# Performance work log

Measured on AMD Instinct MI355X. Metric: run time of the kernel, lower is better.

Reference implementation:

```python
import jax, jax.numpy as jnp
import numpy as np

IOU_THRESHOLD = 0.5


def setup_inputs() -> dict:
    key = jax.random.key(0)
    k1, k2, k3 = jax.random.split(key, 3)
    B, N = 4, 8192
    # valid boxes: top-left in [0,200), width/height in [1,51)
    xy = jax.random.uniform(k1, (B, N, 2), dtype=jnp.float32) * 200.0
    wh = jax.random.uniform(k2, (B, N, 2), dtype=jnp.float32) * 50.0 + 1.0
    boxes = jnp.concatenate([xy, xy + wh], axis=-1)  # [B,N,4] (x1,y1,x2,y2)
    scores = jax.random.uniform(k3, (B, N), dtype=jnp.float32)
    return {"boxes": boxes, "scores": scores}


def _soft_nms_single(boxes, scores):
    # boxes: [N,4], scores: [N]
    x1, y1, x2, y2 = boxes[:, 0], boxes[:, 1], boxes[:, 2], boxes[:, 3]
    inter_w = jnp.maximum(0.0, jnp.minimum(x2[:, None], x2[None, :]) - jnp.maximum(x1[:, None], x1[None, :]))
    inter_h = jnp.maximum(0.0, jnp.minimum(y2[:, None], y2[None, :]) - jnp.maximum(y1[:, None], y1[None, :]))
    inter = inter_w * inter_h  # [N,N]
    area = (x2 - x1) * (y2 - y1)  # [N]
    union = area[:, None] + area[None, :] - inter
    iou = inter / union  # [N,N]
    weight = jnp.exp(-iou / IOU_THRESHOLD)  # [N,N]
    adjusted = weight @ scores  # [N] : adjusted_scores[i] = sum_j w[i,j]*s[j]
    w = jax.nn.softmax(adjusted, axis=0)  # [N]
    return w @ boxes  # [4]


def reference(boxes, scores):
    return jax.vmap(_soft_nms_single)(boxes, scores)  # [B,4]
```

## Files before the change

kernel.cpp:

```cpp
#include <hip/hip_runtime.h>
#include <hip/hip_bf16.h>

#define BATCH   4
#define NBOX    8192
#define BLOCK   256
#define TSZ     256
#define NT      (NBOX / TSZ)
#define NPAIRS  (NT * (NT + 1) / 2)
#define NBINS   2048
#define SUBS    8
#define SUBSZ   (NBOX / SUBS)
#define STH     512

__device__ __forceinline__ float bf2f(unsigned short u) {
    union { unsigned int i; float f; } c;
    c.i = ((unsigned int)u) << 16;
    return c.f;
}

__device__ __forceinline__ bool box_plausible(float x1, float y1, float x2, float y2) {
    bool ok = (x1 == x1) && (y1 == y1) && (x2 == x2) && (y2 == y2);
    ok = ok && fabsf(x1) < 1e4f && fabsf(y1) < 1e4f && fabsf(x2) < 1e4f && fabsf(y2) < 1e4f;
    ok = ok && x1 >= -1.0f && x1 <= 300.0f && y1 >= -1.0f && y1 <= 300.0f;
    const float w = x2 - x1, h = y2 - y1;
    ok = ok && w >= -0.1f && w <= 80.0f && h >= -0.1f && h <= 80.0f;
    return ok;
}

__device__ __forceinline__ bool wave_probe_is_f32(const void* boxes_raw) {
    const int lane = threadIdx.x & 63;
    const float* bf = (const float*)boxes_raw;
    const bool okf = box_plausible(bf[lane * 4 + 0], bf[lane * 4 + 1],
                                   bf[lane * 4 + 2], bf[lane * 4 + 3]);
    const unsigned short* bh = (const unsigned short*)boxes_raw;
    const bool okh = box_plausible(bf2f(bh[lane * 4 + 0]), bf2f(bh[lane * 4 + 1]),
                                   bf2f(bh[lane * 4 + 2]), bf2f(bh[lane * 4 + 3]));
    const unsigned long long mf = __ballot(okf);
    const unsigned long long mh = __ballot(okh);
    return __popcll(mf) >= __popcll(mh);
}

__device__ __forceinline__ float4 load_box(const void* boxes_raw, size_t idx, bool isf32) {
    if (isf32) {
        return reinterpret_cast<const float4*>(boxes_raw)[idx];
    } else {
        const ushort4 u = reinterpret_cast<const ushort4*>(boxes_raw)[idx];
        return make_float4(bf2f(u.x), bf2f(u.y), bf2f(u.z), bf2f(u.w));
    }
}

__device__ __forceinline__ float load_score(const void* scores_raw, size_t idx, bool isf32) {
    return isf32 ? ((const float*)scores_raw)[idx]
                 : bf2f(((const unsigned short*)scores_raw)[idx]);
}

__device__ __forceinline__ int x1_bin(float x1) {
    const int bb = (int)(x1 * 8.0f);
    return min(NBINS - 1, max(0, bb));
}

#define CEXP (-2.8853900817779268f)

__device__ __forceinline__ float pair_weight(
    float ix1, float iy1, float ix2, float iy2, float iarea,
    const float4& bj, float jarea)
{
    float w = fminf(ix2, bj.z) - fmaxf(ix1, bj.x);
    float h = fminf(iy2, bj.w) - fmaxf(iy1, bj.y);
    w = fmaxf(w, 0.0f);
    h = fmaxf(h, 0.0f);
    const float inter = w * h;
    const float uni   = iarea + jarea - inter;
    const float arg   = (CEXP * inter) * __builtin_amdgcn_rcpf(uni);
    return __builtin_amdgcn_exp2f(arg);
}

__global__ __launch_bounds__(STH) void sort_kernel(
    const void* __restrict__ boxes_raw, const void* __restrict__ scores_raw,
    float4* __restrict__ sboxes, float* __restrict__ sscores,
    float* __restrict__ adj,
    float* __restrict__ minx1c, float* __restrict__ maxx2c,
    int* __restrict__ pairlist, int* __restrict__ count)
{
    __shared__ int hist[NBINS];
    __shared__ int bmax[NBINS];
    __shared__ int hist2[NBINS];
    __shared__ int wsum[STH / 64];
    __shared__ float sminT[NT], smaxT[NT];
    __shared__ int scnt;

    const int b    = blockIdx.x / SUBS;
    const int sub  = blockIdx.x % SUBS;
    const int tid  = threadIdx.x;
    const int lane = tid & 63;
    const int wv   = tid >> 6;
    const bool isf32 = wave_probe_is_f32(boxes_raw);
    const size_t base = (size_t)b * NBOX;

#pragma unroll
    for (int i = 0; i < NBINS / STH; i++) {
        hist[i * STH + tid]  = 0;
        bmax[i * STH + tid]  = 0;
        hist2[i * STH + tid] = 0;
    }
    if (tid == 0) scnt = 0;
    {
        const size_t z = (size_t)blockIdx.x * 1024;
        adj[z + tid] = 0.0f;
        adj[z + STH + tid] = 0.0f;
    }
    __syncthreads();

#pragma unroll
    for (int k = 0; k < NBOX / STH; k++) {
        const float4 bx = load_box(boxes_raw, base + k * STH + tid, isf32);
        const int bin = x1_bin(bx.x);
        atomicAdd(&hist[bin], 1);
        atomicMax(&bmax[bin], __float_as_int(bx.z));
    }
    for (int i = tid; i < sub * SUBSZ; i += STH) {
        const float4 bx = load_box(boxes_raw, base + i, isf32);
        atomicAdd(&hist2[x1_bin(bx.x)], 1);
    }
    __syncthreads();

    {
        int tot[4], cum[4];
        int run = 0;
#pragma unroll
        for (int i = 0; i < 4; i++) {
            tot[i] = hist[tid * 4 + i];
            run += tot[i]; cum[i] = run;
        }
        int v = run;
#pragma unroll
        for (int d = 1; d < 64; d <<= 1) {
            const int u = __shfl_up(v, d);
            if (lane >= d) v += u;
        }
        if (lane == 63) wsum[wv] = v;
        __syncthreads();
        int wb = 0;
        for (int w = 0; w < wv; w++) wb += wsum[w];
        const int tb = wb + v - run;
#pragma unroll
        for (int i = 0; i < 4; i++) {
            const int bin = tid * 4 + i;
            const int e = tb + cum[i] - tot[i];
            const int m = hist2[bin];
            hist[bin]  = e;
            hist2[bin] = e + m;
        }
    }
    __syncthreads();

    if (tid < NT) {
        int p = tid * TSZ;
        int lo = 0, hi = NBINS - 1;
        while (lo < hi) { const int mid = (lo + hi + 1) >> 1;
                          if (hist[mid] <= p) lo = mid; else hi = mid - 1; }
        const int Bf = lo;
        p = tid * TSZ + TSZ - 1;
        lo = 0; hi = NBINS - 1;
        while (lo < hi) { const int mid = (lo + hi + 1) >> 1;
                          if (hist[mid] <= p) lo = mid; else hi = mid - 1; }
        const int Bl = lo;
        int mb = 0;
        for (int q = Bf; q <= Bl; q++) mb = max(mb, bmax[q]);
        const float mn = (float)Bf * 0.125f;
        const float mx = __int_as_float(mb);
        sminT[tid] = mn; smaxT[tid] = mx;
        if (sub == 0) {
            minx1c[b * NT + tid] = mn;
            maxx2c[b * NT + tid] = mx;
        }
    }
    __syncthreads();

    if (sub == 0) {
        for (int q = tid; q < NPAIRS; q += STH) {
            int p = q, it = 0;
            while (p >= NT - it) { p -= NT - it; it++; }
            const int jt = it + p;
            const bool live = !((smaxT[it] < sminT[jt]) || (smaxT[jt] < sminT[it]));
            if (live) {
                const int idx = atomicAdd(&scnt, 1);
                pairlist[b * NPAIRS + idx] = (it << 8) | jt;
            }
        }
    }

#pragma unroll
    for (int k = 0; k < SUBSZ / STH; k++) {
        const int i = sub * SUBSZ + k * STH + tid;
        const float4 bx = load_box(boxes_raw, base + i, isf32);
        const float  sc = load_score(scores_raw, base + i, isf32);
        const int pos = atomicAdd(&hist2[x1_bin(bx.x)], 1);
        sboxes[base + pos]  = bx;
        sscores[base + pos] = sc;
    }

    __syncthreads();
    if (sub == 0 && tid == 0) count[b] = scnt;
}

__global__ __launch_bounds__(BLOCK, 4) void soft_nms_adj_kernel(
    const float4* __restrict__ sboxes,
    const float* __restrict__ sscores,
    const int* __restrict__ pairlist,
    const int* __restrict__ count,
    float* __restrict__ adj)
{
    __shared__ float4 sbox[TSZ];
    __shared__ float2 sas[TSZ];
    __shared__ float  srow[4][TSZ];

    const int bid = blockIdx.x;
    const int b   = bid / NPAIRS;
    const int p   = bid % NPAIRS;
    if (p >= count[b]) return;
    const int pr = pairlist[b * NPAIRS + p];
    const int it = pr >> 8, jt = pr & 255;

    const int tid  = threadIdx.x;
    const int lane = tid & 63;
    const int wv   = tid >> 6;
    const size_t base = (size_t)b * NBOX;

    {
        const int jg = jt * TSZ + tid;
        const float4 uj = sboxes[base + jg];
        sbox[tid] = uj;
        sas[tid]  = make_float2((uj.z - uj.x) * (uj.w - uj.y), sscores[base + jg]);
    }

    float rx1[4], ry1[4], rx2[4], ry2[4], rar[4], rsc[4], accr[4];
#pragma unroll
    for (int k = 0; k < 4; k++) {
        const int ig = it * TSZ + k * 64 + lane;
        const float4 ui = sboxes[base + ig];
        rx1[k] = ui.x; ry1[k] = ui.y; rx2[k] = ui.z; ry2[k] = ui.w;
        rar[k] = (ui.z - ui.x) * (ui.w - ui.y);
        rsc[k] = sscores[base + ig];
        accr[k] = 0.0f;
    }

    __syncthreads();

    const int wvbase = wv * 64;

    if (it == jt) {
#pragma unroll 2
        for (int t = 0; t < 64; t++) {
            const int idx = wvbase + ((lane + t) & 63);
            const float4 bj = sbox[idx];
            const float2 as = sas[idx];
#pragma unroll
            for (int k = 0; k < 4; k++) {
                const float e = pair_weight(rx1[k], ry1[k], rx2[k], ry2[k], rar[k], bj, as.x);
                accr[k] = fmaf(e, as.y, accr[k]);
            }
        }
    } else {
        float accc = 0.0f;
#pragma unroll 2
        for (int t = 0; t < 64; t++) {
            const int idx = wvbase + ((lane + t) & 63);
            const float4 bj = sbox[idx];
            const float2 as = sas[idx];
            const float e0 = pair_weight(rx1[0], ry1[0], rx2[0], ry2[0], rar[0], bj, as.x);
            const float e1 = pair_weight(rx1[1], ry1[1], rx2[1], ry2[1], rar[1], bj, as.x);
            const float e2 = pair_weight(rx1[2], ry1[2], rx2[2], ry2[2], rar[2], bj, as.x);
            const float e3 = pair_weight(rx1[3], ry1[3], rx2[3], ry2[3], rar[3], bj, as.x);
            accr[0] = fmaf(e0, as.y, accr[0]);
            accr[1] = fmaf(e1, as.y, accr[1]);
            accr[2] = fmaf(e2, as.y, accr[2]);
            accr[3] = fmaf(e3, as.y, accr[3]);
            const float c = fmaf(e0, rsc[0], fmaf(e1, rsc[1], fmaf(e2, rsc[2], e3 * rsc[3])));
            accc += __shfl(c, (lane - t) & 63);
        }
        atomicAdd(&adj[base + jt * TSZ + wvbase + lane], accc);
    }

#pragma unroll
    for (int k = 0; k < 4; k++) srow[wv][k * 64 + lane] = accr[k];
    __syncthreads();
    {
        const float rs = srow[0][tid] + srow[1][tid] + srow[2][tid] + srow[3][tid];
        atomicAdd(&adj[base + it * TSZ + tid], rs);
    }
}

#define FBLK 1024
__global__ __launch_bounds__(FBLK) void soft_nms_finish_kernel(
    const float4* __restrict__ sboxes,
    const float* __restrict__ sscores,
    const float* __restrict__ adj,
    const float* __restrict__ minx1c, const float* __restrict__ maxx2c,
    const void* __restrict__ boxes_raw,
    void* __restrict__ out)
{
    constexpr int K  = NBOX / FBLK;
    constexpr int NW = FBLK / 64;
    __shared__ float sminx[NT], smaxx[NT], ssumT[NT], scorr[NT];
    __shared__ float smax_[NW];
    __shared__ float sred[NW][5];

    const int b    = blockIdx.x;
    const int tid  = threadIdx.x;
    const int lane = tid & 63;
    const int wv   = tid >> 6;
    const size_t base = (size_t)b * NBOX;

    const bool isf32 = wave_probe_is_f32(boxes_raw);

    if (tid < NT) {
        sminx[tid] = minx1c[b * NT + tid];
        smaxx[tid] = maxx2c[b * NT + tid];
    }
#pragma unroll
    for (int tt = 0; tt < 2; tt++) {
        const int T = wv * 2 + tt;
        float sm = 0.0f;
#pragma unroll
        for (int q = 0; q < 4; q++) sm += sscores[base + T * TSZ + q * 64 + lane];
#pragma unroll
        for (int off = 32; off > 0; off >>= 1) sm += __shfl_down(sm, off);
        if (lane == 0) ssumT[T] = sm;
    }
    __syncthreads();
    if (tid < NT) {
        float c = 0.0f;
        for (int T2 = 0; T2 < NT; T2++) {
            const bool skip = (smaxx[tid] < sminx[T2]) || (smaxx[T2] < sminx[tid]);
            if (skip) c += ssumT[T2];
        }
        scorr[tid] = c;
    }
    __syncthreads();

    float av[K];
    float m = -3.4e38f;
#pragma unroll
    for (int k = 0; k < K; k++) {
        const int r = k * FBLK + tid;
        av[k] = adj[base + r] + scorr[r >> 8];
        m = fmaxf(m, av[k]);
    }
#pragma unroll
    for (int off = 32; off > 0; off >>= 1)
        m = fmaxf(m, __shfl_down(m, off));
    if (lane == 0) smax_[wv] = m;
    __syncthreads();
    float M = smax_[0];
#pragma unroll
    for (int w = 1; w < NW; w++) M = fmaxf(M, smax_[w]);

    const float L2E = 1.4426950408889634f;
    float es = 0.0f, s0 = 0.0f, s1 = 0.0f, s2 = 0.0f, s3 = 0.0f;
#pragma unroll
    for (int k = 0; k < K; k++) {
        const float e = __builtin_amdgcn_exp2f((av[k] - M) * L2E);
        const float4 u = sboxes[base + k * FBLK + tid];
        es += e;
        s0 += e * u.x;
        s1 += e * u.y;
        s2 += e * u.z;
        s3 += e * u.w;
    }
#pragma unroll
    for (int off = 32; off > 0; off >>= 1) {
        es += __shfl_down(es, off);
        s0 += __shfl_down(s0, off);
        s1 += __shfl_down(s1, off);
        s2 += __shfl_down(s2, off);
        s3 += __shfl_down(s3, off);
    }
    if (lane == 0) {
        sred[wv][0] = es; sred[wv][1] = s0; sred[wv][2] = s1;
        sred[wv][3] = s2; sred[wv][4] = s3;
    }
    __syncthreads();
    if (tid == 0) {
        float ES = 0.0f, o[4] = {0.0f, 0.0f, 0.0f, 0.0f};
#pragma unroll
        for (int w = 0; w < NW; w++) {
            ES   += sred[w][0];
            o[0] += sred[w][1];
            o[1] += sred[w][2];
            o[2] += sred[w][3];
            o[3] += sred[w][4];
        }
        const float inv = 1.0f / ES;
        if (isf32) {
            float* of = (float*)out;
            for (int c = 0; c < 4; c++) of[b * 4 + c] = o[c] * inv;
        } else {
            __hip_bfloat16* oh = (__hip_bfloat16*)out;
            for (int c = 0; c < 4; c++) oh[b * 4 + c] = __float2bfloat16(o[c] * inv);
        }
    }
}

extern "C" void kernel_launch(void* const* d_in, const int* in_sizes, int n_in,
                              void* d_out, int out_size, void* d_ws, size_t ws_size,
                              hipStream_t stream) {
    const void* boxes_raw  = d_in[0];
    const void* scores_raw = d_in[1];

    char* w = (char*)d_ws;
    float4* sboxes   = (float4*)w;                 w += (size_t)BATCH * NBOX * 16;
    float*  sscores  = (float*)w;                  w += (size_t)BATCH * NBOX * 4;
    float*  adj      = (float*)w;                  w += (size_t)BATCH * NBOX * 4;
    float*  minx1c   = (float*)w;                  w += (size_t)BATCH * NT * 4;
    float*  maxx2c   = (float*)w;                  w += (size_t)BATCH * NT * 4;
    int*    pairlist = (int*)w;                    w += (size_t)BATCH * NPAIRS * 4;
    int*    count    = (int*)w;

    sort_kernel<<<dim3(BATCH * SUBS), dim3(STH), 0, stream>>>(
        boxes_raw, scores_raw, sboxes, sscores, adj, minx1c, maxx2c, pairlist, count);
    soft_nms_adj_kernel<<<dim3(BATCH * NPAIRS), dim3(BLOCK), 0, stream>>>(
        sboxes, sscores, pairlist, count, adj);
    soft_nms_finish_kernel<<<dim3(BATCH), dim3(FBLK), 0, stream>>>(
        sboxes, sscores, adj, minx1c, maxx2c, boxes_raw, d_out);
}
```

Measured before the change: 120.8 us.

## Fuse sort, pair-adjust and finish stages into one cooperative persistent kernel

Replaces the three-kernel pipeline with one cooperative kernel of 1024 blocks that runs the stages back to back, separated by grid-wide syncs. The sort stage is split into per-sub-block histograms written to global memory, then merged after a grid sync, so the old serial prefix recount is no longer needed. The pair work becomes a persistent loop with 256 blocks per batch, and the finish stage runs in 256-thread blocks. The goal is to remove launch gaps and the long-pole sort prologue; the cost is grid-sync overhead, and only 4 blocks do the final reduction with smaller blocks. The old three-kernel path is kept as a fallback if the cooperative launch fails.

```diff
diff --git a/kernel.cpp b/kernel.cpp
--- a/kernel.cpp
+++ b/kernel.cpp
@@ -1,5 +1,8 @@
 #include <hip/hip_runtime.h>
 #include <hip/hip_bf16.h>
+#include <hip/hip_cooperative_groups.h>
+
+namespace cg = cooperative_groups;
 
 #define BATCH   4
 #define NBOX    8192
@@ -10,7 +13,8 @@
 #define NBINS   2048
 #define SUBS    8
 #define SUBSZ   (NBOX / SUBS)
-#define STH     512
+#define GRID    1024
+#define PPB     256
 
 __device__ __forceinline__ float bf2f(unsigned short u) {
     union { unsigned int i; float f; } c;
@@ -60,6 +64,7 @@
 }
 
 #define CEXP (-2.8853900817779268f)
+#define L2E  (1.4426950408889634f)
 
 __device__ __forceinline__ float pair_weight(
     float ix1, float iy1, float ix2, float iy2, float iarea,
@@ -75,165 +80,17 @@
     return __builtin_amdgcn_exp2f(arg);
 }
 
-__global__ __launch_bounds__(STH) void sort_kernel(
-    const void* __restrict__ boxes_raw, const void* __restrict__ scores_raw,
-    float4* __restrict__ sboxes, float* __restrict__ sscores,
-    float* __restrict__ adj,
-    float* __restrict__ minx1c, float* __restrict__ maxx2c,
-    int* __restrict__ pairlist, int* __restrict__ count)
+__device__ __forceinline__ void adj_pair_body(
+    const float4* sboxes, const float* sscores, float* adj,
+    size_t base, int it, int jt, int tid, int lane, int wv,
+    float4* sbox, float2* sas, float (*srow)[TSZ])
 {
-    __shared__ int hist[NBINS];
-    __shared__ int bmax[NBINS];
-    __shared__ int hist2[NBINS];
-    __shared__ int wsum[STH / 64];
-    __shared__ float sminT[NT], smaxT[NT];
-    __shared__ int scnt;
-
-    const int b    = blockIdx.x / SUBS;
-    const int sub  = blockIdx.x % SUBS;
-    const int tid  = threadIdx.x;
-    const int lane = tid & 63;
-    const int wv   = tid >> 6;
-    const bool isf32 = wave_probe_is_f32(boxes_raw);
-    const size_t base = (size_t)b * NBOX;
-
-#pragma unroll
-    for (int i = 0; i < NBINS / STH; i++) {
-        hist[i * STH + tid]  = 0;
-        bmax[i * STH + tid]  = 0;
-        hist2[i * STH + tid] = 0;
-    }
-    if (tid == 0) scnt = 0;
-    {
-        const size_t z = (size_t)blockIdx.x * 1024;
-        adj[z + tid] = 0.0f;
-        adj[z + STH + tid] = 0.0f;
-    }
-    __syncthreads();
-
-#pragma unroll
-    for (int k = 0; k < NBOX / STH; k++) {
-        const float4 bx = load_box(boxes_raw, base + k * STH + tid, isf32);
-        const int bin = x1_bin(bx.x);
-        atomicAdd(&hist[bin], 1);
-        atomicMax(&bmax[bin], __float_as_int(bx.z));
-    }
-    for (int i = tid; i < sub * SUBSZ; i += STH) {
-        const float4 bx = load_box(boxes_raw, base + i, isf32);
-        atomicAdd(&hist2[x1_bin(bx.x)], 1);
-    }
-    __syncthreads();
-
-    {
-        int tot[4], cum[4];
-        int run = 0;
-#pragma unroll
-        for (int i = 0; i < 4; i++) {
-            tot[i] = hist[tid * 4 + i];
-            run += tot[i]; cum[i] = run;
-        }
-        int v = run;
-#pragma unroll
-        for (int d = 1; d < 64; d <<= 1) {
-            const int u = __shfl_up(v, d);
-            if (lane >= d) v += u;
-        }
-        if (lane == 63) wsum[wv] = v;
-        __syncthreads();
-        int wb = 0;
-        for (int w = 0; w < wv; w++) wb += wsum[w];
-        const int tb = wb + v - run;
-#pragma unroll
-        for (int i = 0; i < 4; i++) {
-            const int bin = tid * 4 + i;
-            const int e = tb + cum[i] - tot[i];
-            const int m = hist2[bin];
-            hist[bin]  = e;
-            hist2[bin] = e + m;
-        }
-    }
-    __syncthreads();
-
-    if (tid < NT) {
-        int p = tid * TSZ;
-        int lo = 0, hi = NBINS - 1;
-        while (lo < hi) { const int mid = (lo + hi + 1) >> 1;
-                          if (hist[mid] <= p) lo = mid; else hi = mid - 1; }
-        const int Bf = lo;
-        p = tid * TSZ + TSZ - 1;
-        lo = 0; hi = NBINS - 1;
-        while (lo < hi) { const int mid = (lo + hi + 1) >> 1;
-                          if (hist[mid] <= p) lo = mid; else hi = mid - 1; }
-        const int Bl = lo;
-        int mb = 0;
-        for (int q = Bf; q <= Bl; q++) mb = max(mb, bmax[q]);
-        const float mn = (float)Bf * 0.125f;
-        const float mx = __int_as_float(mb);
-        sminT[tid] = mn; smaxT[tid] = mx;
-        if (sub == 0) {
-            minx1c[b * NT + tid] = mn;
-            maxx2c[b * NT + tid] = mx;
-        }
-    }
-    __syncthreads();
-
-    if (sub == 0) {
-        for (int q = tid; q < NPAIRS; q += STH) {
-            int p = q, it = 0;
-            while (p >= NT - it) { p -= NT - it; it++; }
-            const int jt = it + p;
-            const bool live = !((smaxT[it] < sminT[jt]) || (smaxT[jt] < sminT[it]));
-            if (live) {
-                const int idx = atomicAdd(&scnt, 1);
-                pairlist[b * NPAIRS + idx] = (it << 8) | jt;
-            }
-        }
-    }
-
-#pragma unroll
-    for (int k = 0; k < SUBSZ / STH; k++) {
-        const int i = sub * SUBSZ + k * STH + tid;
-        const float4 bx = load_box(boxes_raw, base + i, isf32);
-        const float  sc = load_score(scores_raw, base + i, isf32);
-        const int pos = atomicAdd(&hist2[x1_bin(bx.x)], 1);
-        sboxes[base + pos]  = bx;
-        sscores[base + pos] = sc;
-    }
-
-    __syncthreads();
-    if (sub == 0 && tid == 0) count[b] = scnt;
-}
-
-__global__ __launch_bounds__(BLOCK, 4) void soft_nms_adj_kernel(
-    const float4* __restrict__ sboxes,
-    const float* __restrict__ sscores,
-    const int* __restrict__ pairlist,
-    const int* __restrict__ count,
-    float* __restrict__ adj)
-{
-    __shared__ float4 sbox[TSZ];
-    __shared__ float2 sas[TSZ];
-    __shared__ float  srow[4][TSZ];
-
-    const int bid = blockIdx.x;
-    const int b   = bid / NPAIRS;
-    const int p   = bid % NPAIRS;
-    if (p >= count[b]) return;
-    const int pr = pairlist[b * NPAIRS + p];
-    const int it = pr >> 8, jt = pr & 255;
-
-    const int tid  = threadIdx.x;
-    const int lane = tid & 63;
-    const int wv   = tid >> 6;
-    const size_t base = (size_t)b * NBOX;
-
     {
         const int jg = jt * TSZ + tid;
         const float4 uj = sboxes[base + jg];
         sbox[tid] = uj;
         sas[tid]  = make_float2((uj.z - uj.x) * (uj.w - uj.y), sscores[base + jg]);
     }
-
     float rx1[4], ry1[4], rx2[4], ry2[4], rar[4], rsc[4], accr[4];
 #pragma unroll
     for (int k = 0; k < 4; k++) {
@@ -244,11 +101,9 @@
         rsc[k] = sscores[base + ig];
         accr[k] = 0.0f;
     }
-
     __syncthreads();
 
     const int wvbase = wv * 64;
-
     if (it == jt) {
 #pragma unroll 2
         for (int t = 0; t < 64; t++) {
@@ -285,20 +140,397 @@
 #pragma unroll
     for (int k = 0; k < 4; k++) srow[wv][k * 64 + lane] = accr[k];
     __syncthreads();
+    const float rs = srow[0][tid] + srow[1][tid] + srow[2][tid] + srow[3][tid];
+    atomicAdd(&adj[base + it * TSZ + tid], rs);
+}
+
+__global__ __launch_bounds__(BLOCK, 4) void mega_kernel(
+    const void* __restrict__ boxes_raw, const void* __restrict__ scores_raw,
+    float4* __restrict__ sboxes, float* __restrict__ sscores,
+    float* __restrict__ adj,
+    int* __restrict__ ghist, int* __restrict__ gmaxp,
+    float* __restrict__ minx1c, float* __restrict__ maxx2c,
+    int* __restrict__ pairlist, int* __restrict__ count,
+    void* __restrict__ out)
+{
+    cg::grid_group gg = cg::this_grid();
+    __shared__ __align__(16) char smem[25088];
+
+    const int bid  = blockIdx.x;
+    const int tid  = threadIdx.x;
+    const int lane = tid & 63;
+    const int wv   = tid >> 6;
+    const bool isf32 = wave_probe_is_f32(boxes_raw);
+
+    if (bid < BATCH * SUBS) {
+        int* hist = (int*)smem;
+        int* hmax = hist + NBINS;
+        const int b = bid / SUBS, sub = bid % SUBS;
+        const size_t base = (size_t)b * NBOX;
+#pragma unroll
+        for (int i = 0; i < NBINS / BLOCK; i++) {
+            hist[i * BLOCK + tid] = 0; hmax[i * BLOCK + tid] = 0;
+        }
+        __syncthreads();
+#pragma unroll
+        for (int k = 0; k < SUBSZ / BLOCK; k++) {
+            const float4 bx = load_box(boxes_raw, base + sub * SUBSZ + k * BLOCK + tid, isf32);
+            const int bin = x1_bin(bx.x);
+            atomicAdd(&hist[bin], 1);
+            atomicMax(&hmax[bin], __float_as_int(bx.z));
+        }
+        __syncthreads();
+#pragma unroll
+        for (int i = 0; i < NBINS / BLOCK; i++) {
+            const int bin = i * BLOCK + tid;
+            ghist[((size_t)b * NBINS + bin) * SUBS + sub] = hist[bin];
+            gmaxp[((size_t)b * NBINS + bin) * SUBS + sub] = hmax[bin];
+        }
+    } else if (bid < 2 * BATCH * SUBS) {
+        const size_t z = (size_t)(bid - BATCH * SUBS) * 1024;
+#pragma unroll
+        for (int k = 0; k < 4; k++) adj[z + k * BLOCK + tid] = 0.0f;
+    }
+    gg.sync();
+
+    if (bid < BATCH * SUBS) {
+        int*   sex   = (int*)smem;
+        int*   loff  = sex + NBINS;
+        int*   bmaxs = loff + NBINS;
+        int*   wsum  = bmaxs + NBINS;
+        float* sminT = (float*)(wsum + 4);
+        float* smaxT = sminT + NT;
+        int*   scnt  = (int*)(smaxT + NT);
+        const int b = bid / SUBS, sub = bid % SUBS;
+        const size_t base = (size_t)b * NBOX;
+        if (tid == 0) *scnt = 0;
+
+        int tot[8], mys[8], cum[8];
+        int run = 0;
+#pragma unroll
+        for (int i = 0; i < 8; i++) {
+            const int bin = tid * 8 + i;
+            const int* g = &ghist[((size_t)b * NBINS + bin) * SUBS];
+            const int* x = &gmaxp[((size_t)b * NBINS + bin) * SUBS];
+            int t = 0, m = 0, bm = 0;
+#pragma unroll
+            for (int s = 0; s < SUBS; s++) {
+                const int c = g[s];
+                t += c;
+                if (s < sub) m += c;
+                bm = max(bm, x[s]);
+            }
+            tot[i] = t; mys[i] = m; run += t; cum[i] = run;
+            bmaxs[bin] = bm;
+        }
+        int v = run;
+#pragma unroll
+        for (int d = 1; d < 64; d <<= 1) {
+            const int u = __shfl_up(v, d);
+            if (lane >= d) v += u;
+        }
+        if (lane == 63) wsum[wv] = v;
+        __syncthreads();
+        int wb = 0;
+        for (int w2 = 0; w2 < wv; w2++) wb += wsum[w2];
+        const int tb = wb + v - run;
+#pragma unroll
+        for (int i = 0; i < 8; i++) {
+            const int bin = tid * 8 + i;
+            const int e = tb + cum[i] - tot[i];
+            sex[bin]  = e;
+            loff[bin] = e + mys[i];
+        }
+        __syncthreads();
+
+        if (sub == 0 && tid < NT) {
+            int p = tid * TSZ;
+            int lo = 0, hi = NBINS - 1;
+            while (lo < hi) { const int mid = (lo + hi + 1) >> 1;
+                              if (sex[mid] <= p) lo = mid; else hi = mid - 1; }
+            const int Bf = lo;
+            p = tid * TSZ + TSZ - 1;
+            lo = 0; hi = NBINS - 1;
+            while (lo < hi) { const int mid = (lo + hi + 1) >> 1;
+                              if (sex[mid] <= p) lo = mid; else hi = mid - 1; }
+            const int Bl = lo;
+            int mb = 0;
+            for (int q = Bf; q <= Bl; q++) mb = max(mb, bmaxs[q]);
+            sminT[tid] = (float)Bf * 0.125f;
+            smaxT[tid] = __int_as_float(mb);
+            minx1c[b * NT + tid] = sminT[tid];
+            maxx2c[b * NT + tid] = smaxT[tid];
+        }
+        __syncthreads();
+
+        if (sub == 0) {
+            for (int q = tid; q < NPAIRS; q += BLOCK) {
+                int p = q, it = 0;
+                while (p >= NT - it) { p -= NT - it; it++; }
+                const int jt = it + p;
+                const bool live = !((smaxT[it] < sminT[jt]) || (smaxT[jt] < sminT[it]));
+                if (live) {
+                    const int idx = atomicAdd(scnt, 1);
+                    pairlist[b * NPAIRS + idx] = (it << 8) | jt;
+                }
+            }
+        }
+#pragma unroll
+        for (int k = 0; k < SUBSZ / BLOCK; k++) {
+            const int i = sub * SUBSZ + k * BLOCK + tid;
+            const float4 bx = load_box(boxes_raw, base + i, isf32);
+            const float  sc = load_score(scores_raw, base + i, isf32);
+            const int pos = atomicAdd(&loff[x1_bin(bx.x)], 1);
+            sboxes[base + pos]  = bx;
+            sscores[base + pos] = sc;
+        }
+        __syncthreads();
+        if (sub == 0 && tid == 0) count[b] = *scnt;
+    }
+    gg.sync();
+
     {
-        const float rs = srow[0][tid] + srow[1][tid] + srow[2][tid] + srow[3][tid];
-        atomicAdd(&adj[base + it * TSZ + tid], rs);
-    }
+        float4* sbox = (float4*)smem;
+        float2* sas  = (float2*)(smem + 4096);
+        float (*srow)[TSZ] = (float(*)[TSZ])(smem + 6144);
+        const int b  = bid >> 8;
+        const size_t base = (size_t)b * NBOX;
+        const int cnt = count[b];
+        for (int p = (bid & (PPB - 1)); p < cnt; p += PPB) {
+            __syncthreads();
+            const int pr = pairlist[b * NPAIRS + p];
+            adj_pair_body(sboxes, sscores, adj, base, pr >> 8, pr & 255,
+                          tid, lane, wv, sbox, sas, srow);
+        }
+    }
+    gg.sync();
+
+    if (bid < BATCH) {
+        float* sminx = (float*)smem;
+        float* smaxx = sminx + NT;
+        float* ssumT = smaxx + NT;
+        float* scorr = ssumT + NT;
+        float* smaxw = scorr + NT;
+        float (*sred)[5] = (float(*)[5])(smaxw + 4);
+        const int b = bid;
+        const size_t base = (size_t)b * NBOX;
+
+        if (tid < NT) {
+            sminx[tid] = minx1c[b * NT + tid];
+            smaxx[tid] = maxx2c[b * NT + tid];
+        }
+#pragma unroll
+        for (int tt = 0; tt < 8; tt++) {
+            const int T = wv * 8 + tt;
+            float sm = 0.0f;
+#pragma unroll
+            for (int q = 0; q < 4; q++) sm += sscores[base + T * TSZ + q * 64 + lane];
+#pragma unroll
+            for (int off = 32; off > 0; off >>= 1) sm += __shfl_down(sm, off);
+            if (lane == 0) ssumT[T] = sm;
+        }
+        __syncthreads();
+        if (tid < NT) {
+            float c = 0.0f;
+            for (int T2 = 0; T2 < NT; T2++) {
+                const bool skip = (smaxx[tid] < sminx[T2]) || (smaxx[T2] < sminx[tid]);
+                if (skip) c += ssumT[T2];
+            }
+            scorr[tid] = c;
+        }
+        __syncthreads();
+
+        float m = -3.4e38f;
+#pragma unroll
+        for (int k = 0; k < NBOX / BLOCK; k++) {
+            const int r = k * BLOCK + tid;
+            m = fmaxf(m, adj[base + r] + scorr[r >> 8]);
+        }
+#pragma unroll
+        for (int off = 32; off > 0; off >>= 1) m = fmaxf(m, __shfl_down(m, off));
+        if (lane == 0) smaxw[wv] = m;
+        __syncthreads();
+        const float M = fmaxf(fmaxf(smaxw[0], smaxw[1]), fmaxf(smaxw[2], smaxw[3]));
+
+        float es = 0.0f, s0 = 0.0f, s1 = 0.0f, s2 = 0.0f, s3 = 0.0f;
+#pragma unroll
+        for (int k = 0; k < NBOX / BLOCK; k++) {
+            const int r = k * BLOCK + tid;
+            const float e = __builtin_amdgcn_exp2f((adj[base + r] + scorr[r >> 8] - M) * L2E);
+            const float4 u = sboxes[base + r];
+            es += e; s0 += e * u.x; s1 += e * u.y; s2 += e * u.z; s3 += e * u.w;
+        }
+#pragma unroll
+        for (int off = 32; off > 0; off >>= 1) {
+            es += __shfl_down(es, off);
+            s0 += __shfl_down(s0, off);
+            s1 += __shfl_down(s1, off);
+            s2 += __shfl_down(s2, off);
+            s3 += __shfl_down(s3, off);
+        }
+        if (lane == 0) {
+            sred[wv][0] = es; sred[wv][1] = s0; sred[wv][2] = s1;
+            sred[wv][3] = s2; sred[wv][4] = s3;
+        }
+        __syncthreads();
+        if (tid == 0) {
+            float ES = 0.0f, o[4] = {0.0f, 0.0f, 0.0f, 0.0f};
+#pragma unroll
+            for (int w2 = 0; w2 < 4; w2++) {
+                ES += sred[w2][0];
+                o[0] += sred[w2][1]; o[1] += sred[w2][2];
+                o[2] += sred[w2][3]; o[3] += sred[w2][4];
+            }
+            const float inv = 1.0f / ES;
+            if (isf32) {
+                float* of = (float*)out;
+                for (int c = 0; c < 4; c++) of[b * 4 + c] = o[c] * inv;
+            } else {
+                __hip_bfloat16* oh = (__hip_bfloat16*)out;
+                for (int c = 0; c < 4; c++) oh[b * 4 + c] = __float2bfloat16(o[c] * inv);
+            }
+        }
+    }
+}
+
+__global__ __launch_bounds__(512) void sort_kernel_fb(
+    const void* __restrict__ boxes_raw, const void* __restrict__ scores_raw,
+    float4* __restrict__ sboxes, float* __restrict__ sscores,
+    float* __restrict__ adj,
+    float* __restrict__ minx1c, float* __restrict__ maxx2c,
+    int* __restrict__ pairlist, int* __restrict__ count)
+{
+    __shared__ int hist[NBINS];
+    __shared__ int bmax[NBINS];
+    __shared__ int hist2[NBINS];
+    __shared__ int wsum[8];
+    __shared__ float sminT[NT], smaxT[NT];
+    __shared__ int scnt;
+
+    const int b    = blockIdx.x / SUBS;
+    const int sub  = blockIdx.x % SUBS;
+    const int tid  = threadIdx.x;
+    const int lane = tid & 63;
+    const int wv   = tid >> 6;
+    const bool isf32 = wave_probe_is_f32(boxes_raw);
+    const size_t base = (size_t)b * NBOX;
+
+#pragma unroll
+    for (int i = 0; i < NBINS / 512; i++) {
+        hist[i * 512 + tid] = 0; bmax[i * 512 + tid] = 0; hist2[i * 512 + tid] = 0;
+    }
+    if (tid == 0) scnt = 0;
+    {
+        const size_t z = (size_t)blockIdx.x * 1024;
+        adj[z + tid] = 0.0f; adj[z + 512 + tid] = 0.0f;
+    }
+    __syncthreads();
+
+#pragma unroll
+    for (int k = 0; k < NBOX / 512; k++) {
+        const float4 bx = load_box(boxes_raw, base + k * 512 + tid, isf32);
+        const int bin = x1_bin(bx.x);
+        atomicAdd(&hist[bin], 1);
+        atomicMax(&bmax[bin], __float_as_int(bx.z));
+    }
+    for (int i = tid; i < sub * SUBSZ; i += 512) {
+        const float4 bx = load_box(boxes_raw, base + i, isf32);
+        atomicAdd(&hist2[x1_bin(bx.x)], 1);
+    }
+    __syncthreads();
+
+    {
+        int tot[4], cum[4];
+        int run = 0;
+#pragma unroll
+        for (int i = 0; i < 4; i++) { tot[i] = hist[tid * 4 + i]; run += tot[i]; cum[i] = run; }
+        int v = run;
+#pragma unroll
+        for (int d = 1; d < 64; d <<= 1) { const int u = __shfl_up(v, d); if (lane >= d) v += u; }
+        if (lane == 63) wsum[wv] = v;
+        __syncthreads();
+        int wb = 0;
+        for (int w = 0; w < wv; w++) wb += wsum[w];
+        const int tb = wb + v - run;
+#pragma unroll
+        for (int i = 0; i < 4; i++) {
+            const int bin = tid * 4 + i;
+            const int e = tb + cum[i] - tot[i];
+            const int m = hist2[bin];
+            hist[bin]  = e;
+            hist2[bin] = e + m;
+        }
+    }
+    __syncthreads();
+
+    if (tid < NT) {
+        int p = tid * TSZ;
+        int lo = 0, hi = NBINS - 1;
+        while (lo < hi) { const int mid = (lo + hi + 1) >> 1;
+                          if (hist[mid] <= p) lo = mid; else hi = mid - 1; }
+        const int Bf = lo;
+        p = tid * TSZ + TSZ - 1;
+        lo = 0; hi = NBINS - 1;
+        while (lo < hi) { const int mid = (lo + hi + 1) >> 1;
+                          if (hist[mid] <= p) lo = mid; else hi = mid - 1; }
+        const int Bl = lo;
+        int mb = 0;
+        for (int q = Bf; q <= Bl; q++) mb = max(mb, bmax[q]);
+        sminT[tid] = (float)Bf * 0.125f;
+        smaxT[tid] = __int_as_float(mb);
+        if (sub == 0) { minx1c[b * NT + tid] = sminT[tid]; maxx2c[b * NT + tid] = smaxT[tid]; }
+    }
+    __syncthreads();
+
+    if (sub == 0) {
+        for (int q = tid; q < NPAIRS; q += 512) {
+            int p = q, it = 0;
+            while (p >= NT - it) { p -= NT - it; it++; }
+            const int jt = it + p;
+            const bool live = !((smaxT[it] < sminT[jt]) || (smaxT[jt] < sminT[it]));
+            if (live) {
+                const int idx = atomicAdd(&scnt, 1);
+                pairlist[b * NPAIRS + idx] = (it << 8) | jt;
+            }
+        }
+    }
+#pragma unroll
+    for (int k = 0; k < SUBSZ / 512; k++) {
+        const int i = sub * SUBSZ + k * 512 + tid;
+        const float4 bx = load_box(boxes_raw, base + i, isf32);
+        const float  sc = load_score(scores_raw, base + i, isf32);
+        const int pos = atomicAdd(&hist2[x1_bin(bx.x)], 1);
+        sboxes[base + pos]  = bx;
+        sscores[base + pos] = sc;
+    }
+    __syncthreads();
+    if (sub == 0 && tid == 0) count[b] = scnt;
+}
+
+__global__ __launch_bounds__(BLOCK, 4) void adj_kernel_fb(
+    const float4* __restrict__ sboxes, const float* __restrict__ sscores,
+    const int* __restrict__ pairlist, const int* __restrict__ count,
+    float* __restrict__ adj)
+{
+    __shared__ float4 sbox[TSZ];
+    __shared__ float2 sas[TSZ];
+    __shared__ float  srow[4][TSZ];
+
+    const int bid = blockIdx.x;
+    const int b   = bid / NPAIRS;
+    const int p   = bid % NPAIRS;
+    if (p >= count[b]) return;
+    const int pr = pairlist[b * NPAIRS + p];
+    adj_pair_body(sboxes, sscores, adj, (size_t)b * NBOX, pr >> 8, pr & 255,
+                  threadIdx.x, threadIdx.x & 63, threadIdx.x >> 6, sbox, sas, srow);
 }
 
 #define FBLK 1024
-__global__ __launch_bounds__(FBLK) void soft_nms_finish_kernel(
-    const float4* __restrict__ sboxes,
-    const float* __restrict__ sscores,
+__global__ __launch_bounds__(FBLK) void finish_kernel_fb(
+    const float4* __restrict__ sboxes, const float* __restrict__ sscores,
     const float* __restrict__ adj,
     const float* __restrict__ minx1c, const float* __restrict__ maxx2c,
-    const void* __restrict__ boxes_raw,
-    void* __restrict__ out)
+    const void* __restrict__ boxes_raw, void* __restrict__ out)
 {
     constexpr int K  = NBOX / FBLK;
     constexpr int NW = FBLK / 64;
@@ -311,13 +543,9 @@
     const int lane = tid & 63;
     const int wv   = tid >> 6;
     const size_t base = (size_t)b * NBOX;
-
     const bool isf32 = wave_probe_is_f32(boxes_raw);
 
-    if (tid < NT) {
-        sminx[tid] = minx1c[b * NT + tid];
-        smaxx[tid] = maxx2c[b * NT + tid];
-    }
+    if (tid < NT) { sminx[tid] = minx1c[b * NT + tid]; smaxx[tid] = maxx2c[b * NT + tid]; }
 #pragma unroll
     for (int tt = 0; tt < 2; tt++) {
         const int T = wv * 2 + tt;
@@ -348,25 +576,19 @@
         m = fmaxf(m, av[k]);
     }
 #pragma unroll
-    for (int off = 32; off > 0; off >>= 1)
-        m = fmaxf(m, __shfl_down(m, off));
+    for (int off = 32; off > 0; off >>= 1) m = fmaxf(m, __shfl_down(m, off));
     if (lane == 0) smax_[wv] = m;
     __syncthreads();
     float M = smax_[0];
 #pragma unroll
     for (int w = 1; w < NW; w++) M = fmaxf(M, smax_[w]);
 
-    const float L2E = 1.4426950408889634f;
     float es = 0.0f, s0 = 0.0f, s1 = 0.0f, s2 = 0.0f, s3 = 0.0f;
 #pragma unroll
     for (int k = 0; k < K; k++) {
         const float e = __builtin_amdgcn_exp2f((av[k] - M) * L2E);
         const float4 u = sboxes[base + k * FBLK + tid];
-        es += e;
-        s0 += e * u.x;
-        s1 += e * u.y;
-        s2 += e * u.z;
-        s3 += e * u.w;
+        es += e; s0 += e * u.x; s1 += e * u.y; s2 += e * u.z; s3 += e * u.w;
     }
 #pragma unroll
     for (int off = 32; off > 0; off >>= 1) {
@@ -385,11 +607,9 @@
         float ES = 0.0f, o[4] = {0.0f, 0.0f, 0.0f, 0.0f};
 #pragma unroll
         for (int w = 0; w < NW; w++) {
-            ES   += sred[w][0];
-            o[0] += sred[w][1];
-            o[1] += sred[w][2];
-            o[2] += sred[w][3];
-            o[3] += sred[w][4];
+            ES += sred[w][0];
+            o[0] += sred[w][1]; o[1] += sred[w][2];
+            o[2] += sred[w][3]; o[3] += sred[w][4];
         }
         const float inv = 1.0f / ES;
         if (isf32) {
@@ -407,20 +627,32 @@
                               hipStream_t stream) {
     const void* boxes_raw  = d_in[0];
     const void* scores_raw = d_in[1];
+    void* outp = d_out;
 
     char* w = (char*)d_ws;
     float4* sboxes   = (float4*)w;                 w += (size_t)BATCH * NBOX * 16;
     float*  sscores  = (float*)w;                  w += (size_t)BATCH * NBOX * 4;
     float*  adj      = (float*)w;                  w += (size_t)BATCH * NBOX * 4;
+    int*    ghist    = (int*)w;                    w += (size_t)BATCH * NBINS * SUBS * 4;
+    int*    gmaxp    = (int*)w;                    w += (size_t)BATCH * NBINS * SUBS * 4;
     float*  minx1c   = (float*)w;                  w += (size_t)BATCH * NT * 4;
     float*  maxx2c   = (float*)w;                  w += (size_t)BATCH * NT * 4;
     int*    pairlist = (int*)w;                    w += (size_t)BATCH * NPAIRS * 4;
     int*    count    = (int*)w;
 
-    sort_kernel<<<dim3(BATCH * SUBS), dim3(STH), 0, stream>>>(
-        boxes_raw, scores_raw, sboxes, sscores, adj, minx1c, maxx2c, pairlist, count);
-    soft_nms_adj_kernel<<<dim3(BATCH * NPAIRS), dim3(BLOCK), 0, stream>>>(
-        sboxes, sscores, pairlist, count, adj);
-    soft_nms_finish_kernel<<<dim3(BATCH), dim3(FBLK), 0, stream>>>(
-        sboxes, sscores, adj, minx1c, maxx2c, boxes_raw, d_out);
-}
+    void* kargs[] = { (void*)&boxes_raw, (void*)&scores_raw, (void*)&sboxes,
+                      (void*)&sscores, (void*)&adj, (void*)&ghist, (void*)&gmaxp,
+                      (void*)&minx1c, (void*)&maxx2c, (void*)&pairlist,
+                      (void*)&count, (void*)&outp };
+    const hipError_t err = hipLaunchCooperativeKernel(
+        (const void*)mega_kernel, dim3(GRID), dim3(BLOCK), kargs, 0, stream);
+    if (err != hipSuccess) {
+        (void)hipGetLastError();
+        sort_kernel_fb<<<dim3(BATCH * SUBS), dim3(512), 0, stream>>>(
+            boxes_raw, scores_raw, sboxes, sscores, adj, minx1c, maxx2c, pairlist, count);
+        adj_kernel_fb<<<dim3(BATCH * NPAIRS), dim3(BLOCK), 0, stream>>>(
+            sboxes, sscores, pairlist, count, adj);
+        finish_kernel_fb<<<dim3(BATCH), dim3(FBLK), 0, stream>>>(
+            sboxes, sscores, adj, minx1c, maxx2c, boxes_raw, outp);
+    }
+}
```

New measurement: 415.6 us. +244.0%, slower.

## Sort tiles by y inside block and skip non-overlapping 64-box sub-tile pairs

Applied to the files above, without the earlier changes.

Each tile pair now sorts its i and j boxes by y1 with an in-shared-memory rank sort. It computes per-wave y ranges and score sums, then skips 64x64 sub-blocks whose y ranges cannot overlap. For skipped sub-blocks the weight is taken as exp(0)=1, so their contribution is added as a plain score sum. Results are scattered back through permutation arrays. This cuts the exp/IoU work for pairs that cannot intersect, at the cost of an O(256) rank sort per tile, extra syncs, and shared memory that may reduce occupancy.

```diff
diff --git a/kernel.cpp b/kernel.cpp
--- a/kernel.cpp
+++ b/kernel.cpp
@@ -204,6 +204,28 @@
     if (sub == 0 && tid == 0) count[b] = scnt;
 }
 
+template<int N, bool DIAG>
+__device__ __forceinline__ void run_tloop(
+    const float4* sbj, const float2* saj, int wvbase, int lane,
+    const float* rx1, const float* ry1, const float* rx2, const float* ry2,
+    const float* rar, const float* rsc, float* accr, float& accc)
+{
+#pragma unroll 2
+    for (int t = 0; t < 64; t++) {
+        const int idx = wvbase + ((lane + t) & 63);
+        const float4 bj = sbj[idx];
+        const float2 as = saj[idx];
+        float c = 0.0f;
+#pragma unroll
+        for (int q = 0; q < N; q++) {
+            const float e = pair_weight(rx1[q], ry1[q], rx2[q], ry2[q], rar[q], bj, as.x);
+            accr[q] = fmaf(e, as.y, accr[q]);
+            if (!DIAG) c = fmaf(e, rsc[q], c);
+        }
+        if (!DIAG) accc += __shfl(c, (lane - t) & 63);
+    }
+}
+
 __global__ __launch_bounds__(BLOCK, 4) void soft_nms_adj_kernel(
     const float4* __restrict__ sboxes,
     const float* __restrict__ sscores,
@@ -211,9 +233,13 @@
     const int* __restrict__ count,
     float* __restrict__ adj)
 {
-    __shared__ float4 sbox[TSZ];
-    __shared__ float2 sas[TSZ];
-    __shared__ float  srow[4][TSZ];
+    __shared__ float4 sbi[TSZ];
+    __shared__ float2 sai[TSZ];
+    __shared__ float4 sbj[TSZ];
+    __shared__ float2 saj[TSZ];
+    __shared__ int    permi[TSZ], permj[TSZ];
+    __shared__ __align__(16) float tmpbuf[1536];
+    __shared__ float ymini[4], ymaxi[4], yminj[4], ymaxj[4], rsumi[4], rsumj[4];
 
     const int bid = blockIdx.x;
     const int b   = bid / NPAIRS;
@@ -228,66 +254,126 @@
     const size_t base = (size_t)b * NBOX;
 
     {
-        const int jg = jt * TSZ + tid;
-        const float4 uj = sboxes[base + jg];
-        sbox[tid] = uj;
-        sas[tid]  = make_float2((uj.z - uj.x) * (uj.w - uj.y), sscores[base + jg]);
-    }
+        float* ytmp = tmpbuf + 1280;
+        {
+            const float4 bx = sboxes[base + it * TSZ + tid];
+            const float  sc = sscores[base + it * TSZ + tid];
+            ytmp[tid] = bx.y;
+            __syncthreads();
+            int rank = 0;
+            const float yt = bx.y;
+#pragma unroll 8
+            for (int j = 0; j < TSZ; j++) {
+                const float yj = ytmp[j];
+                rank += (yj < yt) || (yj == yt && j < tid);
+            }
+            sbi[rank]   = bx;
+            sai[rank]   = make_float2((bx.z - bx.x) * (bx.w - bx.y), sc);
+            permi[rank] = tid;
+            __syncthreads();
+        }
+        {
+            const float4 bx = sboxes[base + jt * TSZ + tid];
+            const float  sc = sscores[base + jt * TSZ + tid];
+            ytmp[tid] = bx.y;
+            __syncthreads();
+            int rank = 0;
+            const float yt = bx.y;
+#pragma unroll 8
+            for (int j = 0; j < TSZ; j++) {
+                const float yj = ytmp[j];
+                rank += (yj < yt) || (yj == yt && j < tid);
+            }
+            sbj[rank]   = bx;
+            saj[rank]   = make_float2((bx.z - bx.x) * (bx.w - bx.y), sc);
+            permj[rank] = tid;
+            __syncthreads();
+        }
+    }
+
+    const int wvbase = wv * 64;
+
+    {
+        float y2i = sbi[wvbase + lane].w;
+        float y2j = sbj[wvbase + lane].w;
+        float ssi = sai[wvbase + lane].y;
+        float ssj = saj[wvbase + lane].y;
+#pragma unroll
+        for (int off = 32; off > 0; off >>= 1) {
+            y2i = fmaxf(y2i, __shfl_down(y2i, off));
+            y2j = fmaxf(y2j, __shfl_down(y2j, off));
+            ssi += __shfl_down(ssi, off);
+            ssj += __shfl_down(ssj, off);
+        }
+        if (lane == 0) {
+            ymaxi[wv] = y2i; ymaxj[wv] = y2j;
+            rsumi[wv] = ssi; rsumj[wv] = ssj;
+            ymini[wv] = sbi[wvbase].y;
+            yminj[wv] = sbj[wvbase].y;
+        }
+    }
+    __syncthreads();
+
+    int mask = 0;
+    float ccorr = 0.0f;
+#pragma unroll
+    for (int k = 0; k < 4; k++) {
+        const bool live = (ymini[k] <= ymaxj[wv]) && (yminj[wv] <= ymaxi[k]);
+        if (live) mask |= (1 << k);
+        else      ccorr += rsumi[k];
+    }
+    const int nl = __popc(mask);
+    int m2 = mask;
+    const int l0 = __ffs(m2) - 1; m2 &= m2 - 1;
+    const int l1 = __ffs(m2) - 1; m2 &= m2 - 1;
+    const int l2 = __ffs(m2) - 1; m2 &= m2 - 1;
+    const int l3 = __ffs(m2) - 1;
 
     float rx1[4], ry1[4], rx2[4], ry2[4], rar[4], rsc[4], accr[4];
+    accr[0] = accr[1] = accr[2] = accr[3] = 0.0f;
+#define LOADSLOT(q, lk)                                                      \
+    if (nl > (q)) {                                                          \
+        const int r = (lk) * 64 + lane;                                      \
+        const float4 u = sbi[r]; const float2 a = sai[r];                    \
+        rx1[q] = u.x; ry1[q] = u.y; rx2[q] = u.z; ry2[q] = u.w;              \
+        rar[q] = a.x; rsc[q] = a.y;                                          \
+    }
+    LOADSLOT(0, l0) LOADSLOT(1, l1) LOADSLOT(2, l2) LOADSLOT(3, l3)
+#undef LOADSLOT
+
+    float accc = ccorr;
+    if (it != jt) {
+        switch (nl) {
+            case 4: run_tloop<4,false>(sbj, saj, wvbase, lane, rx1,ry1,rx2,ry2,rar,rsc, accr, accc); break;
+            case 3: run_tloop<3,false>(sbj, saj, wvbase, lane, rx1,ry1,rx2,ry2,rar,rsc, accr, accc); break;
+            case 2: run_tloop<2,false>(sbj, saj, wvbase, lane, rx1,ry1,rx2,ry2,rar,rsc, accr, accc); break;
+            case 1: run_tloop<1,false>(sbj, saj, wvbase, lane, rx1,ry1,rx2,ry2,rar,rsc, accr, accc); break;
+            default: break;
+        }
+        atomicAdd(&adj[base + jt * TSZ + permj[wvbase + lane]], accc);
+    } else {
+        switch (nl) {
+            case 4: run_tloop<4,true>(sbj, saj, wvbase, lane, rx1,ry1,rx2,ry2,rar,rsc, accr, accc); break;
+            case 3: run_tloop<3,true>(sbj, saj, wvbase, lane, rx1,ry1,rx2,ry2,rar,rsc, accr, accc); break;
+            case 2: run_tloop<2,true>(sbj, saj, wvbase, lane, rx1,ry1,rx2,ry2,rar,rsc, accr, accc); break;
+            case 1: run_tloop<1,true>(sbj, saj, wvbase, lane, rx1,ry1,rx2,ry2,rar,rsc, accr, accc); break;
+            default: break;
+        }
+    }
+
+    float (*srow)[TSZ] = (float(*)[TSZ])tmpbuf;
+    if (nl > 0) srow[wv][l0 * 64 + lane] = accr[0];
+    if (nl > 1) srow[wv][l1 * 64 + lane] = accr[1];
+    if (nl > 2) srow[wv][l2 * 64 + lane] = accr[2];
+    if (nl > 3) srow[wv][l3 * 64 + lane] = accr[3];
 #pragma unroll
     for (int k = 0; k < 4; k++) {
-        const int ig = it * TSZ + k * 64 + lane;
-        const float4 ui = sboxes[base + ig];
-        rx1[k] = ui.x; ry1[k] = ui.y; rx2[k] = ui.z; ry2[k] = ui.w;
-        rar[k] = (ui.z - ui.x) * (ui.w - ui.y);
-        rsc[k] = sscores[base + ig];
-        accr[k] = 0.0f;
-    }
-
-    __syncthreads();
-
-    const int wvbase = wv * 64;
-
-    if (it == jt) {
-#pragma unroll 2
-        for (int t = 0; t < 64; t++) {
-            const int idx = wvbase + ((lane + t) & 63);
-            const float4 bj = sbox[idx];
-            const float2 as = sas[idx];
-#pragma unroll
-            for (int k = 0; k < 4; k++) {
-                const float e = pair_weight(rx1[k], ry1[k], rx2[k], ry2[k], rar[k], bj, as.x);
-                accr[k] = fmaf(e, as.y, accr[k]);
-            }
-        }
-    } else {
-        float accc = 0.0f;
-#pragma unroll 2
-        for (int t = 0; t < 64; t++) {
-            const int idx = wvbase + ((lane + t) & 63);
-            const float4 bj = sbox[idx];
-            const float2 as = sas[idx];
-            const float e0 = pair_weight(rx1[0], ry1[0], rx2[0], ry2[0], rar[0], bj, as.x);
-            const float e1 = pair_weight(rx1[1], ry1[1], rx2[1], ry2[1], rar[1], bj, as.x);
-            const float e2 = pair_weight(rx1[2], ry1[2], rx2[2], ry2[2], rar[2], bj, as.x);
-            const float e3 = pair_weight(rx1[3], ry1[3], rx2[3], ry2[3], rar[3], bj, as.x);
-            accr[0] = fmaf(e0, as.y, accr[0]);
-            accr[1] = fmaf(e1, as.y, accr[1]);
-            accr[2] = fmaf(e2, as.y, accr[2]);
-            accr[3] = fmaf(e3, as.y, accr[3]);
-            const float c = fmaf(e0, rsc[0], fmaf(e1, rsc[1], fmaf(e2, rsc[2], e3 * rsc[3])));
-            accc += __shfl(c, (lane - t) & 63);
-        }
-        atomicAdd(&adj[base + jt * TSZ + wvbase + lane], accc);
-    }
-
-#pragma unroll
-    for (int k = 0; k < 4; k++) srow[wv][k * 64 + lane] = accr[k];
+        if (!(mask & (1 << k))) srow[wv][k * 64 + lane] = rsumj[wv];
+    }
     __syncthreads();
     {
         const float rs = srow[0][tid] + srow[1][tid] + srow[2][tid] + srow[3][tid];
-        atomicAdd(&adj[base + it * TSZ + tid], rs);
+        atomicAdd(&adj[base + it * TSZ + permi[tid]], rs);
     }
 }
 
```

After: 138.5 us. 1.15x slower.
